# Optimization experiments

Measured on AMD Instinct MI355X. Metric: run time of the kernel, lower is better.

The kernel has to match this reference:

```python
import jax, jax.numpy as jnp
import numpy as np

B, CQ, CK, CV, CO = 16, 256, 256, 256, 256
H, W = 80, 80          # query spatial size (P3-like)
KH, KW = 40, 40        # key/value spatial size (P4-like)
HEADS = 4
R2 = 2 * 2             # region_size ** 2
SCALE = 1.0 / np.float32(np.sqrt(CQ))


def conv1x1(x, w, b):
    # 1x1 conv == per-pixel linear map over channels
    return jnp.einsum('bchw,oc->bohw', x, w) + b[None, :, None, None]


def setup_inputs() -> dict:
    key = jax.random.key(0)
    ks = jax.random.split(key, 10)
    s = 0.05
    return {
        'query': jax.random.normal(ks[0], (B, CQ, H, W), jnp.float32),
        'key':   jax.random.normal(ks[1], (B, CK, KH, KW), jnp.float32),
        'wq': jax.random.normal(ks[2], (CQ, CQ), jnp.float32) * s,
        'bq': jax.random.normal(ks[3], (CQ,), jnp.float32) * s,
        'wk': jax.random.normal(ks[4], (CK, CK), jnp.float32) * s,
        'bk': jax.random.normal(ks[5], (CK,), jnp.float32) * s,
        'wv': jax.random.normal(ks[6], (CV, CV), jnp.float32) * s,
        'bv': jax.random.normal(ks[7], (CV,), jnp.float32) * s,
        'wo': jax.random.normal(ks[8], (CO, CV), jnp.float32) * s,
        'bo': jax.random.normal(ks[9], (CO,), jnp.float32) * s,
    }


def reference(query, key, wq, bq, wk, bk, wv, bv, wo, bo):
    # value defaults to key in the original module
    q = conv1x1(query, wq, bq)               # [B,CQ,H,W]
    k = conv1x1(key, wk, bk)                 # [B,CK,KH,KW]
    v = conv1x1(key, wv, bv)                 # [B,CV,KH,KW]

    b, cq, h, w = q.shape
    # All R2 'patches' in the source are the SAME interpolation (no offsets),
    # so compute it once; bilinear resize matches torch align_corners=False.
    ki = jax.image.resize(k, (b, k.shape[1], h, w), method='bilinear')
    vi = jax.image.resize(v, (b, v.shape[1], h, w), method='bilinear')

    q5 = q.reshape(b, HEADS, cq // HEADS, h, w)
    k5 = ki.reshape(b, HEADS, k.shape[1] // HEADS, h, w)
    v5 = vi.reshape(b, HEADS, v.shape[1] // HEADS, h, w)

    # per-region score; identical for every region patch
    score = jnp.einsum('bhcxy,bhcxy->bhxy', q5, k5) * SCALE     # [B,h,H,W]
    scores = jnp.broadcast_to(score[:, :, None], (b, HEADS, R2, h, w))
    # NOTE: original uses nn.Softmax(dim=3) -> normalizes over the H axis
    attn = jax.nn.softmax(scores, axis=3)                       # [B,h,R2,H,W]

    # out = sum over regions of attn * v (v identical across regions)
    out = jnp.einsum('bhrxy,bhcxy->bhcxy', attn, v5)            # [B,h,C/h,H,W]
    out = out.reshape(b, -1, h, w)                              # [B,CV,H,W]
    return conv1x1(out, wo, bo)                                 # [B,CO,H,W]
```

## Files before the change

### kernel.cpp

```cpp
#include <hip/hip_runtime.h>
#include <hip/hip_bf16.h>

typedef __bf16 bf16;
typedef __attribute__((ext_vector_type(4))) float f32x4;
typedef __attribute__((ext_vector_type(8))) __bf16 bf16x8;
typedef __attribute__((ext_vector_type(4))) __bf16 bf16x4;

__global__ __launch_bounds__(256, 2)
void gemm_cm(const float* __restrict__ act, const float* __restrict__ W,
             const float* __restrict__ bias, bf16* __restrict__ out, int P) {
  __shared__ alignas(16) bf16 At[128][64];
  __shared__ alignas(16) bf16 Bt[128][64];
  const int t = threadIdx.x;
  const int b = blockIdx.z;
  const int m0 = blockIdx.x * 128;
  const int n0 = blockIdx.y * 128;
  const int w = t >> 6, l = t & 63;
  const int wr = w >> 1, wc = w & 1;
  const int lrow = l & 15, koff = (l >> 4) * 8;

  const float* actb = act + (size_t)b * 256 * (size_t)P;

  f32x4 acc[4][4];
#pragma unroll
  for (int i = 0; i < 4; ++i)
#pragma unroll
    for (int j = 0; j < 4; ++j) acc[i][j] = (f32x4){0.f, 0.f, 0.f, 0.f};

  for (int kt = 0; kt < 4; ++kt) {
    const int k0 = kt * 64;
    if (kt) __syncthreads();
#pragma unroll
    for (int u = 0; u < 2; ++u) {
      int unit = u * 256 + t;
      int up = unit & 31;
      int uk = unit >> 5;
      int ps = m0 + up * 4;
      if (ps > P - 4) ps = P - 4;
      f32x4 r0 = *(const f32x4*)(actb + (size_t)(k0 + uk * 4 + 0) * P + ps);
      f32x4 r1 = *(const f32x4*)(actb + (size_t)(k0 + uk * 4 + 1) * P + ps);
      f32x4 r2 = *(const f32x4*)(actb + (size_t)(k0 + uk * 4 + 2) * P + ps);
      f32x4 r3 = *(const f32x4*)(actb + (size_t)(k0 + uk * 4 + 3) * P + ps);
      int cs = (uk * 4) ^ ((up & 7) << 3);
#pragma unroll
      for (int j = 0; j < 4; ++j) {
        bf16x4 v = {(bf16)r0[j], (bf16)r1[j], (bf16)r2[j], (bf16)r3[j]};
        *(bf16x4*)&At[up * 4 + j][cs] = v;
      }
    }
#pragma unroll
    for (int it = 0; it < 8; ++it) {
      int idx = it * 256 + t;
      int row = idx >> 4, ce = (idx & 15) * 4;
      f32x4 v = *(const f32x4*)(W + (size_t)(n0 + row) * 256 + k0 + ce);
      bf16x4 h = {(bf16)v[0], (bf16)v[1], (bf16)v[2], (bf16)v[3]};
      *(bf16x4*)&Bt[row][ce] = h;
    }
    __syncthreads();

#pragma unroll
    for (int kk = 0; kk < 2; ++kk) {
      bf16x8 af[4], bv[4];
#pragma unroll
      for (int i = 0; i < 4; ++i) {
        int ar = wr * 64 + i * 16 + lrow;
        int kb = kk * 32 + koff;
        af[i] = *(const bf16x8*)&At[ar][kb ^ (((ar >> 2) & 7) << 3)];
        bv[i] = *(const bf16x8*)&Bt[wc * 64 + i * 16 + lrow][kb];
      }
#pragma unroll
      for (int mi = 0; mi < 4; ++mi)
#pragma unroll
        for (int ni = 0; ni < 4; ++ni)
          acc[mi][ni] = __builtin_amdgcn_mfma_f32_16x16x32_bf16(af[mi], bv[ni], acc[mi][ni], 0, 0, 0);
    }
  }

  bf16* ob = out + (size_t)b * (size_t)P * 256;
#pragma unroll
  for (int mi = 0; mi < 4; ++mi) {
#pragma unroll
    for (int r = 0; r < 4; ++r) {
      int p_ = m0 + wr * 64 + mi * 16 + (l >> 4) * 4 + r;
      if (p_ < P) {
#pragma unroll
        for (int ni = 0; ni < 4; ++ni) {
          int o_ = n0 + wc * 64 + ni * 16 + (l & 15);
          ob[(size_t)p_ * 256 + o_] = (bf16)(acc[mi][ni][r] + bias[o_]);
        }
      }
    }
  }
}

__global__ __launch_bounds__(256, 2)
void gemm_pm(const bf16* __restrict__ act, const float* __restrict__ W,
             const float* __restrict__ bias, float* __restrict__ out, int P) {
  __shared__ alignas(16) bf16 At[128][64];
  __shared__ alignas(16) bf16 Bt[128][64];
  const int t = threadIdx.x;
  const int b = blockIdx.z;
  const int m0 = blockIdx.x * 128;
  const int n0 = blockIdx.y * 128;
  const int w = t >> 6, l = t & 63;
  const int wr = w >> 1, wc = w & 1;
  const int lrow = l & 15, koff = (l >> 4) * 8;

  const bf16* actb = act + (size_t)b * (size_t)P * 256;

  f32x4 acc[4][4];
#pragma unroll
  for (int i = 0; i < 4; ++i)
#pragma unroll
    for (int j = 0; j < 4; ++j) acc[i][j] = (f32x4){0.f, 0.f, 0.f, 0.f};

  for (int kt = 0; kt < 4; ++kt) {
    const int k0 = kt * 64;
    if (kt) __syncthreads();
#pragma unroll
    for (int it = 0; it < 8; ++it) {
      int idx = it * 256 + t;
      int row = idx >> 4, ce = (idx & 15) * 4;
      f32x4 v = *(const f32x4*)(W + (size_t)(m0 + row) * 256 + k0 + ce);
      bf16x4 h = {(bf16)v[0], (bf16)v[1], (bf16)v[2], (bf16)v[3]};
      *(bf16x4*)&At[row][ce] = h;
    }
#pragma unroll
    for (int it = 0; it < 4; ++it) {
      int idx = it * 256 + t;
      int row = idx >> 3, ce = (idx & 7) * 8;
      bf16x8 v = *(const bf16x8*)(actb + (size_t)(n0 + row) * 256 + k0 + ce);
      *(bf16x8*)&Bt[row][ce] = v;
    }
    __syncthreads();

#pragma unroll
    for (int kk = 0; kk < 2; ++kk) {
      bf16x8 af[4], bv[4];
#pragma unroll
      for (int i = 0; i < 4; ++i) {
        af[i] = *(const bf16x8*)&At[wr * 64 + i * 16 + lrow][kk * 32 + koff];
        bv[i] = *(const bf16x8*)&Bt[wc * 64 + i * 16 + lrow][kk * 32 + koff];
      }
#pragma unroll
      for (int mi = 0; mi < 4; ++mi)
#pragma unroll
        for (int ni = 0; ni < 4; ++ni)
          acc[mi][ni] = __builtin_amdgcn_mfma_f32_16x16x32_bf16(af[mi], bv[ni], acc[mi][ni], 0, 0, 0);
    }
  }

  float* ob = out + (size_t)b * 256 * (size_t)P;
#pragma unroll
  for (int mi = 0; mi < 4; ++mi) {
#pragma unroll
    for (int r = 0; r < 4; ++r) {
      int o_ = m0 + wr * 64 + mi * 16 + (l >> 4) * 4 + r;
      float bvf = bias[o_];
#pragma unroll
      for (int ni = 0; ni < 4; ++ni) {
        int p_ = n0 + wc * 64 + ni * 16 + (l & 15);
        ob[(size_t)o_ * P + p_] = acc[mi][ni][r] + bvf;
      }
    }
  }
}

__global__ void score_kernel(const bf16* __restrict__ Qpm, const bf16* __restrict__ Kpm,
                             float* __restrict__ score) {
  const int t = threadIdx.x;
  const int p = blockIdx.x * 256 + t;
  const int hd = blockIdx.y, b = blockIdx.z;
  const int x = p / 80, y = p % 80;

  float cx = 0.5f * x - 0.25f;
  int ix = (int)floorf(cx);
  float wx1 = cx - ix;
  int x0 = ix < 0 ? 0 : ix, x1 = (ix + 1 > 39) ? 39 : ix + 1;
  float cy = 0.5f * y - 0.25f;
  int iy = (int)floorf(cy);
  float wy1 = cy - iy;
  int y0 = iy < 0 ? 0 : iy, y1 = (iy + 1 > 39) ? 39 : iy + 1;
  float w00 = (1.f - wx1) * (1.f - wy1), w01 = (1.f - wx1) * wy1;
  float w10 = wx1 * (1.f - wy1), w11 = wx1 * wy1;

  const bf16* q   = Qpm + ((size_t)b * 6400 + p) * 256 + hd * 64;
  const bf16* k00 = Kpm + ((size_t)b * 1600 + x0 * 40 + y0) * 256 + hd * 64;
  const bf16* k01 = Kpm + ((size_t)b * 1600 + x0 * 40 + y1) * 256 + hd * 64;
  const bf16* k10 = Kpm + ((size_t)b * 1600 + x1 * 40 + y0) * 256 + hd * 64;
  const bf16* k11 = Kpm + ((size_t)b * 1600 + x1 * 40 + y1) * 256 + hd * 64;

  float dot = 0.f;
#pragma unroll
  for (int i = 0; i < 8; ++i) {
    bf16x8 qv = *(const bf16x8*)(q + i * 8);
    bf16x8 a = *(const bf16x8*)(k00 + i * 8);
    bf16x8 c = *(const bf16x8*)(k01 + i * 8);
    bf16x8 d = *(const bf16x8*)(k10 + i * 8);
    bf16x8 e = *(const bf16x8*)(k11 + i * 8);
#pragma unroll
    for (int j = 0; j < 8; ++j) {
      float kup = w00 * (float)a[j] + w01 * (float)c[j] + w10 * (float)d[j] + w11 * (float)e[j];
      dot += (float)qv[j] * kup;
    }
  }
  score[((size_t)b * 4 + hd) * 6400 + p] = dot * 0.0625f;
}

__global__ void smax_kernel(float* __restrict__ score) {
  __shared__ float s[6400];
  const int hd = blockIdx.x, b = blockIdx.y, t = threadIdx.x;
  float* buf = score + ((size_t)b * 4 + hd) * 6400;
  for (int i = t; i < 6400; i += 256) s[i] = buf[i];
  __syncthreads();
  if (t < 80) {
    const int y = t;
    float m = -1e30f;
    for (int x = 0; x < 80; ++x) m = fmaxf(m, s[x * 80 + y]);
    float sum = 0.f;
    for (int x = 0; x < 80; ++x) {
      float e = __expf(s[x * 80 + y] - m);
      s[x * 80 + y] = e;
      sum += e;
    }
    float inv = 4.0f / sum;
    for (int x = 0; x < 80; ++x) buf[x * 80 + y] = s[x * 80 + y] * inv;
  }
}

__global__ void outgen_kernel(const bf16* __restrict__ Vpm, const float* __restrict__ attn,
                              bf16* __restrict__ outpm) {
  __shared__ float Vx[40][256];
  __shared__ float at[4][80];
  const int x = blockIdx.x, b = blockIdx.y, t = threadIdx.x;

  float cx = 0.5f * x - 0.25f;
  int ix = (int)floorf(cx);
  float wx1 = cx - ix, wx0 = 1.f - wx1;
  int tx0 = ix < 0 ? 0 : ix, tx1 = (ix + 1 > 39) ? 39 : ix + 1;

  const bf16* r0 = Vpm + ((size_t)b * 1600 + tx0 * 40) * 256;
  const bf16* r1 = Vpm + ((size_t)b * 1600 + tx1 * 40) * 256;
  for (int ty = 0; ty < 40; ++ty)
    Vx[ty][t] = wx0 * (float)r0[ty * 256 + t] + wx1 * (float)r1[ty * 256 + t];
  for (int i = t; i < 320; i += 256) {
    int hd = i / 80, y = i % 80;
    at[hd][y] = attn[((size_t)b * 4 + hd) * 6400 + x * 80 + y];
  }
  __syncthreads();

  const int hd = t >> 6;
  bf16* ob = outpm + ((size_t)b * 6400 + x * 80) * 256;
  for (int y = 0; y < 80; ++y) {
    float cyv = 0.5f * y - 0.25f;
    int iy = (int)floorf(cyv);
    float wy1 = cyv - iy;
    int ty0 = iy < 0 ? 0 : iy, ty1 = (iy + 1 > 39) ? 39 : iy + 1;
    float v = (1.f - wy1) * Vx[ty0][t] + wy1 * Vx[ty1][t];
    ob[(size_t)y * 256 + t] = (bf16)(at[hd][y] * v);
  }
}

extern "C" void kernel_launch(void* const* d_in, const int* in_sizes, int n_in,
                              void* d_out, int out_size, void* d_ws, size_t ws_size,
                              hipStream_t stream) {
  const float* query = (const float*)d_in[0];
  const float* key   = (const float*)d_in[1];
  const float* wq    = (const float*)d_in[2];
  const float* bq    = (const float*)d_in[3];
  const float* wk    = (const float*)d_in[4];
  const float* bk    = (const float*)d_in[5];
  const float* wv    = (const float*)d_in[6];
  const float* bv    = (const float*)d_in[7];
  const float* wo    = (const float*)d_in[8];
  const float* bo    = (const float*)d_in[9];

  char* ws = (char*)d_ws;
  bf16*  outpm = (bf16*)(ws);
  bf16*  Kpm   = (bf16*)(ws + 52428800);
  bf16*  Vpm   = (bf16*)(ws + 65536000);
  float* score = (float*)(ws + 78643200);
  bf16*  Qpm   = (bf16*)d_out;

  gemm_cm<<<dim3(50, 2, 16), 256, 0, stream>>>(query, wq, bq, Qpm, 6400);
  gemm_cm<<<dim3(13, 2, 16), 256, 0, stream>>>(key, wk, bk, Kpm, 1600);
  gemm_cm<<<dim3(13, 2, 16), 256, 0, stream>>>(key, wv, bv, Vpm, 1600);
  score_kernel<<<dim3(25, 4, 16), 256, 0, stream>>>(Qpm, Kpm, score);
  smax_kernel<<<dim3(4, 16), 256, 0, stream>>>(score);
  outgen_kernel<<<dim3(80, 16), 256, 0, stream>>>(Vpm, score, outpm);
  gemm_pm<<<dim3(2, 50, 16), 256, 0, stream>>>(outpm, wo, bo, (float*)d_out, 6400);
}
```

Baseline: 208.5 us.

## Fuse Q projection with score, merge KV GEMMs, pre-convert weights, double-buffer GEMMs

Weights are converted to bf16 once in a small pre-kernel. The K and V projections now run in one launch, and their epilogue is staged through shared memory so global stores are coalesced. The Q projection is fused with the bilinear score computation, so the Qpm intermediate is never written to or read from global memory. All GEMMs move to 512-thread blocks with double-buffered LDS, direct global-to-LDS loads and XOR swizzling, and the output GEMM writes vectorized stores. The costs are lower occupancy (one block per CU), a single-use extra launch per call, and only half the threads doing work in the fused score epilogue.

```diff
diff --git a/kernel.cpp b/kernel.cpp
--- a/kernel.cpp
+++ b/kernel.cpp
@@ -6,205 +6,274 @@
 typedef __attribute__((ext_vector_type(8))) __bf16 bf16x8;
 typedef __attribute__((ext_vector_type(4))) __bf16 bf16x4;
 
-__global__ __launch_bounds__(256, 2)
-void gemm_cm(const float* __restrict__ act, const float* __restrict__ W,
-             const float* __restrict__ bias, bf16* __restrict__ out, int P) {
-  __shared__ alignas(16) bf16 At[128][64];
-  __shared__ alignas(16) bf16 Bt[128][64];
+static __device__ __forceinline__ void gl16(const void* g, void* l) {
+  __builtin_amdgcn_global_load_lds((const __attribute__((address_space(1))) void*)g,
+                                   (__attribute__((address_space(3))) void*)l, 16, 0, 0);
+}
+static __device__ __forceinline__ bf16x8 frag(const bf16* tile, int row, int kb) {
+  return *(const bf16x8*)(tile + row * 64 + ((((kb) >> 3) ^ (row & 7)) << 3));
+}
+
+__global__ void wpre(const float* __restrict__ w0, const float* __restrict__ w1,
+                     const float* __restrict__ w2, const float* __restrict__ w3,
+                     bf16* __restrict__ dst) {
+  const float* srcs[4] = {w0, w1, w2, w3};
+  const float* s = srcs[blockIdx.y];
+  bf16* d = dst + (size_t)blockIdx.y * 65536;
+  int base = blockIdx.x * 2048 + threadIdx.x * 8;
+  f32x4 a = *(const f32x4*)(s + base);
+  f32x4 b = *(const f32x4*)(s + base + 4);
+  bf16x8 v = {(bf16)a[0], (bf16)a[1], (bf16)a[2], (bf16)a[3],
+              (bf16)b[0], (bf16)b[1], (bf16)b[2], (bf16)b[3]};
+  *(bf16x8*)(d + base) = v;
+}
+
+__global__ __launch_bounds__(512, 1)
+void qgemm_score(const float* __restrict__ query, const bf16* __restrict__ Wq,
+                 const float* __restrict__ bq, const bf16* __restrict__ Kpm,
+                 float* __restrict__ score) {
+  __shared__ alignas(16) char smem[65536];
   const int t = threadIdx.x;
   const int b = blockIdx.z;
   const int m0 = blockIdx.x * 128;
   const int n0 = blockIdx.y * 128;
   const int w = t >> 6, l = t & 63;
-  const int wr = w >> 1, wc = w & 1;
+  const int wr = w & 1, wc = w >> 1;
   const int lrow = l & 15, koff = (l >> 4) * 8;
-
-  const float* actb = act + (size_t)b * 256 * (size_t)P;
-
-  f32x4 acc[4][4];
+  const int up = t & 31, uk = t >> 5;
+  const float* actb = query + (size_t)b * 256 * 6400;
+
+  f32x4 Ar[4];
+  f32x4 acc[4][2];
 #pragma unroll
   for (int i = 0; i < 4; ++i)
 #pragma unroll
-    for (int j = 0; j < 4; ++j) acc[i][j] = (f32x4){0.f, 0.f, 0.f, 0.f};
-
+    for (int j = 0; j < 2; ++j) acc[i][j] = (f32x4){0.f, 0.f, 0.f, 0.f};
+
+  auto Ab = [&](int buf) { return (bf16*)(smem + buf * 16384); };
+  auto Bb = [&](int buf) { return (bf16*)(smem + 32768 + buf * 16384); };
+
+  auto GLOADB = [&](int kt, int buf) {
+    const int k0 = kt * 64;
+#pragma unroll
+    for (int call = 0; call < 2; ++call) {
+      int idx = call * 512 + t;
+      int row = idx >> 3, u = idx & 7;
+      gl16(Wq + (size_t)(n0 + row) * 256 + k0 + ((u ^ (row & 7)) << 3), Bb(buf) + idx * 8);
+    }
+  };
+  auto ALOAD = [&](int kt) {
+    const int k0 = kt * 64;
+    int ps = m0 + up * 4;
+#pragma unroll
+    for (int j = 0; j < 4; ++j)
+      Ar[j] = *(const f32x4*)(actb + (size_t)(k0 + uk * 4 + j) * 6400 + ps);
+  };
+  auto ASTORE = [&](int buf) {
+#pragma unroll
+    for (int j = 0; j < 4; ++j) {
+      int row = up * 4 + j;
+      int cs = (uk * 4) ^ ((row & 7) << 3);
+      bf16x4 v = {(bf16)Ar[0][j], (bf16)Ar[1][j], (bf16)Ar[2][j], (bf16)Ar[3][j]};
+      *(bf16x4*)(Ab(buf) + row * 64 + cs) = v;
+    }
+  };
+  auto COMPUTE = [&](int buf) {
+#pragma unroll
+    for (int kk = 0; kk < 2; ++kk) {
+      const int kb = kk * 32 + koff;
+      bf16x8 af[4], bv[2];
+#pragma unroll
+      for (int i = 0; i < 4; ++i) af[i] = frag(Ab(buf), wr * 64 + i * 16 + lrow, kb);
+#pragma unroll
+      for (int j = 0; j < 2; ++j) bv[j] = frag(Bb(buf), wc * 32 + j * 16 + lrow, kb);
+#pragma unroll
+      for (int i = 0; i < 4; ++i)
+#pragma unroll
+        for (int j = 0; j < 2; ++j)
+          acc[i][j] = __builtin_amdgcn_mfma_f32_16x16x32_bf16(af[i], bv[j], acc[i][j], 0, 0, 0);
+    }
+  };
+
+  GLOADB(0, 0);
+  ALOAD(0);
+  ASTORE(0);
+  __syncthreads();
+#pragma unroll
   for (int kt = 0; kt < 4; ++kt) {
-    const int k0 = kt * 64;
-    if (kt) __syncthreads();
-#pragma unroll
-    for (int u = 0; u < 2; ++u) {
-      int unit = u * 256 + t;
-      int up = unit & 31;
-      int uk = unit >> 5;
-      int ps = m0 + up * 4;
-      if (ps > P - 4) ps = P - 4;
-      f32x4 r0 = *(const f32x4*)(actb + (size_t)(k0 + uk * 4 + 0) * P + ps);
-      f32x4 r1 = *(const f32x4*)(actb + (size_t)(k0 + uk * 4 + 1) * P + ps);
-      f32x4 r2 = *(const f32x4*)(actb + (size_t)(k0 + uk * 4 + 2) * P + ps);
-      f32x4 r3 = *(const f32x4*)(actb + (size_t)(k0 + uk * 4 + 3) * P + ps);
-      int cs = (uk * 4) ^ ((up & 7) << 3);
-#pragma unroll
-      for (int j = 0; j < 4; ++j) {
-        bf16x4 v = {(bf16)r0[j], (bf16)r1[j], (bf16)r2[j], (bf16)r3[j]};
-        *(bf16x4*)&At[up * 4 + j][cs] = v;
+    const int cur = kt & 1;
+    if (kt < 3) { GLOADB(kt + 1, cur ^ 1); ALOAD(kt + 1); }
+    __builtin_amdgcn_sched_barrier(0);
+    COMPUTE(cur);
+    if (kt < 3) ASTORE(cur ^ 1);
+    __syncthreads();
+  }
+
+  bf16* Qs = (bf16*)smem;
+#pragma unroll
+  for (int mi = 0; mi < 4; ++mi) {
+#pragma unroll
+    for (int ni = 0; ni < 2; ++ni) {
+      int ch = wc * 32 + ni * 16 + (l & 15);
+      float bvf = bq[n0 + ch];
+#pragma unroll
+      for (int r = 0; r < 4; ++r) {
+        int p = wr * 64 + mi * 16 + (l >> 4) * 4 + r;
+        Qs[p * 136 + ch] = (bf16)(acc[mi][ni][r] + bvf);
       }
     }
-#pragma unroll
-    for (int it = 0; it < 8; ++it) {
-      int idx = it * 256 + t;
-      int row = idx >> 4, ce = (idx & 15) * 4;
-      f32x4 v = *(const f32x4*)(W + (size_t)(n0 + row) * 256 + k0 + ce);
-      bf16x4 h = {(bf16)v[0], (bf16)v[1], (bf16)v[2], (bf16)v[3]};
-      *(bf16x4*)&Bt[row][ce] = h;
-    }
-    __syncthreads();
-
-#pragma unroll
-    for (int kk = 0; kk < 2; ++kk) {
-      bf16x8 af[4], bv[4];
-#pragma unroll
-      for (int i = 0; i < 4; ++i) {
-        int ar = wr * 64 + i * 16 + lrow;
-        int kb = kk * 32 + koff;
-        af[i] = *(const bf16x8*)&At[ar][kb ^ (((ar >> 2) & 7) << 3)];
-        bv[i] = *(const bf16x8*)&Bt[wc * 64 + i * 16 + lrow][kb];
+  }
+  __syncthreads();
+
+  if (t < 256) {
+    int pl = t & 127, hl = t >> 7;
+    int hd = (n0 >> 6) + hl;
+    int p = m0 + pl;
+    int x = p / 80, y = p % 80;
+    float cx = 0.5f * x - 0.25f;
+    int ix = (int)floorf(cx);
+    float wx1 = cx - ix;
+    int x0 = ix < 0 ? 0 : ix, x1 = (ix + 1 > 39) ? 39 : ix + 1;
+    float cy = 0.5f * y - 0.25f;
+    int iy = (int)floorf(cy);
+    float wy1 = cy - iy;
+    int y0 = iy < 0 ? 0 : iy, y1 = (iy + 1 > 39) ? 39 : iy + 1;
+    float w00 = (1.f - wx1) * (1.f - wy1), w01 = (1.f - wx1) * wy1;
+    float w10 = wx1 * (1.f - wy1), w11 = wx1 * wy1;
+    const bf16* k00 = Kpm + ((size_t)b * 1600 + x0 * 40 + y0) * 256 + hd * 64;
+    const bf16* k01 = Kpm + ((size_t)b * 1600 + x0 * 40 + y1) * 256 + hd * 64;
+    const bf16* k10 = Kpm + ((size_t)b * 1600 + x1 * 40 + y0) * 256 + hd * 64;
+    const bf16* k11 = Kpm + ((size_t)b * 1600 + x1 * 40 + y1) * 256 + hd * 64;
+    float dot = 0.f;
+#pragma unroll
+    for (int i = 0; i < 8; ++i) {
+      bf16x8 qv = *(const bf16x8*)(Qs + pl * 136 + hl * 64 + i * 8);
+      bf16x8 a = *(const bf16x8*)(k00 + i * 8);
+      bf16x8 c = *(const bf16x8*)(k01 + i * 8);
+      bf16x8 d = *(const bf16x8*)(k10 + i * 8);
+      bf16x8 e = *(const bf16x8*)(k11 + i * 8);
+#pragma unroll
+      for (int j = 0; j < 8; ++j) {
+        float kup = w00 * (float)a[j] + w01 * (float)c[j] + w10 * (float)d[j] + w11 * (float)e[j];
+        dot += (float)qv[j] * kup;
       }
-#pragma unroll
-      for (int mi = 0; mi < 4; ++mi)
-#pragma unroll
-        for (int ni = 0; ni < 4; ++ni)
-          acc[mi][ni] = __builtin_amdgcn_mfma_f32_16x16x32_bf16(af[mi], bv[ni], acc[mi][ni], 0, 0, 0);
-    }
-  }
-
-  bf16* ob = out + (size_t)b * (size_t)P * 256;
-#pragma unroll
-  for (int mi = 0; mi < 4; ++mi) {
-#pragma unroll
-    for (int r = 0; r < 4; ++r) {
-      int p_ = m0 + wr * 64 + mi * 16 + (l >> 4) * 4 + r;
-      if (p_ < P) {
-#pragma unroll
-        for (int ni = 0; ni < 4; ++ni) {
-          int o_ = n0 + wc * 64 + ni * 16 + (l & 15);
-          ob[(size_t)p_ * 256 + o_] = (bf16)(acc[mi][ni][r] + bias[o_]);
-        }
-      }
-    }
-  }
-}
-
-__global__ __launch_bounds__(256, 2)
-void gemm_pm(const bf16* __restrict__ act, const float* __restrict__ W,
-             const float* __restrict__ bias, float* __restrict__ out, int P) {
-  __shared__ alignas(16) bf16 At[128][64];
-  __shared__ alignas(16) bf16 Bt[128][64];
+    }
+    score[((size_t)b * 4 + hd) * 6400 + p] = dot * 0.0625f;
+  }
+}
+
+__global__ __launch_bounds__(512, 1)
+void kv_gemm(const float* __restrict__ key,
+             const bf16* __restrict__ Wk, const float* __restrict__ bk, bf16* __restrict__ Kpm,
+             const bf16* __restrict__ Wv, const float* __restrict__ bv, bf16* __restrict__ Vpm) {
+  __shared__ alignas(16) char smem[65536];
+  const int P = 1600;
   const int t = threadIdx.x;
   const int b = blockIdx.z;
   const int m0 = blockIdx.x * 128;
-  const int n0 = blockIdx.y * 128;
+  const int sel = blockIdx.y >> 1;
+  const int n0 = (blockIdx.y & 1) * 128;
+  const bf16* W = sel ? Wv : Wk;
+  const float* bias = sel ? bv : bk;
+  bf16* out = sel ? Vpm : Kpm;
   const int w = t >> 6, l = t & 63;
-  const int wr = w >> 1, wc = w & 1;
+  const int wr = w & 1, wc = w >> 1;
   const int lrow = l & 15, koff = (l >> 4) * 8;
-
-  const bf16* actb = act + (size_t)b * (size_t)P * 256;
-
-  f32x4 acc[4][4];
+  const int up = t & 31, uk = t >> 5;
+  const float* actb = key + (size_t)b * 256 * P;
+
+  f32x4 Ar[4];
+  f32x4 acc[4][2];
 #pragma unroll
   for (int i = 0; i < 4; ++i)
 #pragma unroll
-    for (int j = 0; j < 4; ++j) acc[i][j] = (f32x4){0.f, 0.f, 0.f, 0.f};
-
+    for (int j = 0; j < 2; ++j) acc[i][j] = (f32x4){0.f, 0.f, 0.f, 0.f};
+
+  auto Ab = [&](int buf) { return (bf16*)(smem + buf * 16384); };
+  auto Bb = [&](int buf) { return (bf16*)(smem + 32768 + buf * 16384); };
+
+  auto GLOADB = [&](int kt, int buf) {
+    const int k0 = kt * 64;
+#pragma unroll
+    for (int call = 0; call < 2; ++call) {
+      int idx = call * 512 + t;
+      int row = idx >> 3, u = idx & 7;
+      gl16(W + (size_t)(n0 + row) * 256 + k0 + ((u ^ (row & 7)) << 3), Bb(buf) + idx * 8);
+    }
+  };
+  auto ALOAD = [&](int kt) {
+    const int k0 = kt * 64;
+    int ps = m0 + up * 4;
+    if (ps > P - 4) ps = P - 4;
+#pragma unroll
+    for (int j = 0; j < 4; ++j)
+      Ar[j] = *(const f32x4*)(actb + (size_t)(k0 + uk * 4 + j) * P + ps);
+  };
+  auto ASTORE = [&](int buf) {
+#pragma unroll
+    for (int j = 0; j < 4; ++j) {
+      int row = up * 4 + j;
+      int cs = (uk * 4) ^ ((row & 7) << 3);
+      bf16x4 v = {(bf16)Ar[0][j], (bf16)Ar[1][j], (bf16)Ar[2][j], (bf16)Ar[3][j]};
+      *(bf16x4*)(Ab(buf) + row * 64 + cs) = v;
+    }
+  };
+  auto COMPUTE = [&](int buf) {
+#pragma unroll
+    for (int kk = 0; kk < 2; ++kk) {
+      const int kb = kk * 32 + koff;
+      bf16x8 af[4], bvv[2];
+#pragma unroll
+      for (int i = 0; i < 4; ++i) af[i] = frag(Ab(buf), wr * 64 + i * 16 + lrow, kb);
+#pragma unroll
+      for (int j = 0; j < 2; ++j) bvv[j] = frag(Bb(buf), wc * 32 + j * 16 + lrow, kb);
+#pragma unroll
+      for (int i = 0; i < 4; ++i)
+#pragma unroll
+        for (int j = 0; j < 2; ++j)
+          acc[i][j] = __builtin_amdgcn_mfma_f32_16x16x32_bf16(af[i], bvv[j], acc[i][j], 0, 0, 0);
+    }
+  };
+
+  GLOADB(0, 0);
+  ALOAD(0);
+  ASTORE(0);
+  __syncthreads();
+#pragma unroll
   for (int kt = 0; kt < 4; ++kt) {
-    const int k0 = kt * 64;
-    if (kt) __syncthreads();
-#pragma unroll
-    for (int it = 0; it < 8; ++it) {
-      int idx = it * 256 + t;
-      int row = idx >> 4, ce = (idx & 15) * 4;
-      f32x4 v = *(const f32x4*)(W + (size_t)(m0 + row) * 256 + k0 + ce);
-      bf16x4 h = {(bf16)v[0], (bf16)v[1], (bf16)v[2], (bf16)v[3]};
-      *(bf16x4*)&At[row][ce] = h;
-    }
-#pragma unroll
-    for (int it = 0; it < 4; ++it) {
-      int idx = it * 256 + t;
-      int row = idx >> 3, ce = (idx & 7) * 8;
-      bf16x8 v = *(const bf16x8*)(actb + (size_t)(n0 + row) * 256 + k0 + ce);
-      *(bf16x8*)&Bt[row][ce] = v;
-    }
+    const int cur = kt & 1;
+    if (kt < 3) { GLOADB(kt + 1, cur ^ 1); ALOAD(kt + 1); }
+    __builtin_amdgcn_sched_barrier(0);
+    COMPUTE(cur);
+    if (kt < 3) ASTORE(cur ^ 1);
     __syncthreads();
-
-#pragma unroll
-    for (int kk = 0; kk < 2; ++kk) {
-      bf16x8 af[4], bv[4];
-#pragma unroll
-      for (int i = 0; i < 4; ++i) {
-        af[i] = *(const bf16x8*)&At[wr * 64 + i * 16 + lrow][kk * 32 + koff];
-        bv[i] = *(const bf16x8*)&Bt[wc * 64 + i * 16 + lrow][kk * 32 + koff];
+  }
+
+  bf16* Sc = (bf16*)smem;
+#pragma unroll
+  for (int mi = 0; mi < 4; ++mi) {
+#pragma unroll
+    for (int ni = 0; ni < 2; ++ni) {
+      int ch = wc * 32 + ni * 16 + (l & 15);
+      float bvf = bias[n0 + ch];
+#pragma unroll
+      for (int r = 0; r < 4; ++r) {
+        int p = wr * 64 + mi * 16 + (l >> 4) * 4 + r;
+        Sc[p * 136 + ch] = (bf16)(acc[mi][ni][r] + bvf);
       }
-#pragma unroll
-      for (int mi = 0; mi < 4; ++mi)
-#pragma unroll
-        for (int ni = 0; ni < 4; ++ni)
-          acc[mi][ni] = __builtin_amdgcn_mfma_f32_16x16x32_bf16(af[mi], bv[ni], acc[mi][ni], 0, 0, 0);
-    }
-  }
-
-  float* ob = out + (size_t)b * 256 * (size_t)P;
-#pragma unroll
-  for (int mi = 0; mi < 4; ++mi) {
-#pragma unroll
-    for (int r = 0; r < 4; ++r) {
-      int o_ = m0 + wr * 64 + mi * 16 + (l >> 4) * 4 + r;
-      float bvf = bias[o_];
-#pragma unroll
-      for (int ni = 0; ni < 4; ++ni) {
-        int p_ = n0 + wc * 64 + ni * 16 + (l & 15);
-        ob[(size_t)o_ * P + p_] = acc[mi][ni][r] + bvf;
-      }
-    }
-  }
-}
-
-__global__ void score_kernel(const bf16* __restrict__ Qpm, const bf16* __restrict__ Kpm,
-                             float* __restrict__ score) {
-  const int t = threadIdx.x;
-  const int p = blockIdx.x * 256 + t;
-  const int hd = blockIdx.y, b = blockIdx.z;
-  const int x = p / 80, y = p % 80;
-
-  float cx = 0.5f * x - 0.25f;
-  int ix = (int)floorf(cx);
-  float wx1 = cx - ix;
-  int x0 = ix < 0 ? 0 : ix, x1 = (ix + 1 > 39) ? 39 : ix + 1;
-  float cy = 0.5f * y - 0.25f;
-  int iy = (int)floorf(cy);
-  float wy1 = cy - iy;
-  int y0 = iy < 0 ? 0 : iy, y1 = (iy + 1 > 39) ? 39 : iy + 1;
-  float w00 = (1.f - wx1) * (1.f - wy1), w01 = (1.f - wx1) * wy1;
-  float w10 = wx1 * (1.f - wy1), w11 = wx1 * wy1;
-
-  const bf16* q   = Qpm + ((size_t)b * 6400 + p) * 256 + hd * 64;
-  const bf16* k00 = Kpm + ((size_t)b * 1600 + x0 * 40 + y0) * 256 + hd * 64;
-  const bf16* k01 = Kpm + ((size_t)b * 1600 + x0 * 40 + y1) * 256 + hd * 64;
-  const bf16* k10 = Kpm + ((size_t)b * 1600 + x1 * 40 + y0) * 256 + hd * 64;
-  const bf16* k11 = Kpm + ((size_t)b * 1600 + x1 * 40 + y1) * 256 + hd * 64;
-
-  float dot = 0.f;
-#pragma unroll
-  for (int i = 0; i < 8; ++i) {
-    bf16x8 qv = *(const bf16x8*)(q + i * 8);
-    bf16x8 a = *(const bf16x8*)(k00 + i * 8);
-    bf16x8 c = *(const bf16x8*)(k01 + i * 8);
-    bf16x8 d = *(const bf16x8*)(k10 + i * 8);
-    bf16x8 e = *(const bf16x8*)(k11 + i * 8);
-#pragma unroll
-    for (int j = 0; j < 8; ++j) {
-      float kup = w00 * (float)a[j] + w01 * (float)c[j] + w10 * (float)d[j] + w11 * (float)e[j];
-      dot += (float)qv[j] * kup;
-    }
-  }
-  score[((size_t)b * 4 + hd) * 6400 + p] = dot * 0.0625f;
+    }
+  }
+  __syncthreads();
+  bf16* ob = out + (size_t)b * P * 256;
+#pragma unroll
+  for (int pass = 0; pass < 4; ++pass) {
+    int unit = pass * 512 + t;
+    int row = unit >> 4, cu = unit & 15;
+    if (m0 + row < P) {
+      bf16x8 v = *(const bf16x8*)(Sc + row * 136 + cu * 8);
+      *(bf16x8*)(ob + (size_t)(m0 + row) * 256 + n0 + cu * 8) = v;
+    }
+  }
 }
 
 __global__ void smax_kernel(float* __restrict__ score) {
@@ -258,6 +327,81 @@
     int ty0 = iy < 0 ? 0 : iy, ty1 = (iy + 1 > 39) ? 39 : iy + 1;
     float v = (1.f - wy1) * Vx[ty0][t] + wy1 * Vx[ty1][t];
     ob[(size_t)y * 256 + t] = (bf16)(at[hd][y] * v);
+  }
+}
+
+__global__ __launch_bounds__(512, 1)
+void gemm_out(const bf16* __restrict__ act, const bf16* __restrict__ Wo,
+              const float* __restrict__ bias, float* __restrict__ out) {
+  __shared__ alignas(16) char smem[65536];
+  const int t = threadIdx.x;
+  const int b = blockIdx.z;
+  const int m0 = blockIdx.x * 128;
+  const int n0 = blockIdx.y * 128;
+  const int w = t >> 6, l = t & 63;
+  const int wr = w & 1, wc = w >> 1;
+  const int lrow = l & 15, koff = (l >> 4) * 8;
+  const bf16* actb = act + (size_t)b * 6400 * 256;
+
+  f32x4 acc[4][2];
+#pragma unroll
+  for (int i = 0; i < 4; ++i)
+#pragma unroll
+    for (int j = 0; j < 2; ++j) acc[i][j] = (f32x4){0.f, 0.f, 0.f, 0.f};
+
+  auto Ab = [&](int buf) { return (bf16*)(smem + buf * 16384); };
+  auto Bb = [&](int buf) { return (bf16*)(smem + 32768 + buf * 16384); };
+
+  auto GLOADS = [&](int kt, int buf) {
+    const int k0 = kt * 64;
+#pragma unroll
+    for (int call = 0; call < 2; ++call) {
+      int idx = call * 512 + t;
+      int row = idx >> 3, u = idx & 7;
+      gl16(actb + (size_t)(m0 + row) * 256 + k0 + ((u ^ (row & 7)) << 3), Ab(buf) + idx * 8);
+      gl16(Wo + (size_t)(n0 + row) * 256 + k0 + ((u ^ (row & 7)) << 3), Bb(buf) + idx * 8);
+    }
+  };
+  auto COMPUTE = [&](int buf) {
+#pragma unroll
+    for (int kk = 0; kk < 2; ++kk) {
+      const int kb = kk * 32 + koff;
+      bf16x8 af[4], bvv[2];
+#pragma unroll
+      for (int i = 0; i < 4; ++i) af[i] = frag(Ab(buf), wr * 64 + i * 16 + lrow, kb);
+#pragma unroll
+      for (int j = 0; j < 2; ++j) bvv[j] = frag(Bb(buf), wc * 32 + j * 16 + lrow, kb);
+#pragma unroll
+      for (int i = 0; i < 4; ++i)
+#pragma unroll
+        for (int j = 0; j < 2; ++j)
+          acc[i][j] = __builtin_amdgcn_mfma_f32_16x16x32_bf16(af[i], bvv[j], acc[i][j], 0, 0, 0);
+    }
+  };
+
+  GLOADS(0, 0);
+  __syncthreads();
+#pragma unroll
+  for (int kt = 0; kt < 4; ++kt) {
+    const int cur = kt & 1;
+    if (kt < 3) GLOADS(kt + 1, cur ^ 1);
+    __builtin_amdgcn_sched_barrier(0);
+    COMPUTE(cur);
+    __syncthreads();
+  }
+
+  float* ob = out + (size_t)b * 256 * 6400;
+#pragma unroll
+  for (int mi = 0; mi < 4; ++mi) {
+    int pbase = m0 + wr * 64 + mi * 16 + (l >> 4) * 4;
+#pragma unroll
+    for (int ni = 0; ni < 2; ++ni) {
+      int o_ = n0 + wc * 32 + ni * 16 + (l & 15);
+      float bvf = bias[o_];
+      f32x4 v = {acc[mi][ni][0] + bvf, acc[mi][ni][1] + bvf,
+                 acc[mi][ni][2] + bvf, acc[mi][ni][3] + bvf};
+      *(f32x4*)(ob + (size_t)o_ * 6400 + pbase) = v;
+    }
   }
 }
 
@@ -280,13 +424,13 @@
   bf16*  Kpm   = (bf16*)(ws + 52428800);
   bf16*  Vpm   = (bf16*)(ws + 65536000);
   float* score = (float*)(ws + 78643200);
-  bf16*  Qpm   = (bf16*)d_out;
-
-  gemm_cm<<<dim3(50, 2, 16), 256, 0, stream>>>(query, wq, bq, Qpm, 6400);
-  gemm_cm<<<dim3(13, 2, 16), 256, 0, stream>>>(key, wk, bk, Kpm, 1600);
-  gemm_cm<<<dim3(13, 2, 16), 256, 0, stream>>>(key, wv, bv, Vpm, 1600);
-  score_kernel<<<dim3(25, 4, 16), 256, 0, stream>>>(Qpm, Kpm, score);
+  bf16*  Wb    = (bf16*)(ws + 85196800);
+  bf16* wqb = Wb, *wkb = Wb + 65536, *wvb = Wb + 131072, *wob = Wb + 196608;
+
+  wpre<<<dim3(32, 4), 256, 0, stream>>>(wq, wk, wv, wo, Wb);
+  kv_gemm<<<dim3(13, 4, 16), 512, 0, stream>>>(key, wkb, bk, Kpm, wvb, bv, Vpm);
+  qgemm_score<<<dim3(50, 2, 16), 512, 0, stream>>>(query, wqb, bq, Kpm, score);
   smax_kernel<<<dim3(4, 16), 256, 0, stream>>>(score);
   outgen_kernel<<<dim3(80, 16), 256, 0, stream>>>(Vpm, score, outpm);
-  gemm_pm<<<dim3(2, 50, 16), 256, 0, stream>>>(outpm, wo, bo, (float*)d_out, 6400);
-}
+  gemm_out<<<dim3(50, 2, 16), 512, 0, stream>>>(outpm, wob, bo, (float*)d_out);
+}
```

After: 179.6 us. 13.9% less time.
